# Kernel optimization log

Hardware: AMD Instinct MI355X
Metric: run time of the kernel (lower is better)

The kernel has to match this reference:

```python
import jax, jax.numpy as jnp
import numpy as np

N_AGENTS, RNN_H, N_HEADS, GAT_D, EMB, SDIM = 16, 64, 4, 32, 32, 128


def setup_inputs() -> dict:
    key = jax.random.key(0)
    ks = jax.random.split(key, 16)
    xav = lambda k, shp: jax.random.normal(k, shp, jnp.float32) * (2.0 / sum(shp)) ** 0.5
    return {
        'agent_qs': jax.random.normal(ks[0], (32, 128, N_AGENTS), jnp.float32),
        'states': jax.random.normal(ks[1], (32, 128, SDIM), jnp.float32),
        'hidden_states': jax.random.normal(ks[2], (32, 128, N_AGENTS, RNN_H), jnp.float32),
        'uncertainty': jax.random.uniform(ks[3], (32, 128, 1), jnp.float32),
        'W_gat': xav(ks[4], (RNN_H, N_HEADS * GAT_D)) * 1.414,
        'att_a': xav(ks[5], (1, N_HEADS, 2 * GAT_D)) * 1.414,
        'w1s_W': xav(ks[6], (SDIM + 1, N_HEADS * EMB * GAT_D)),
        'w1s_b': jnp.zeros((N_HEADS * EMB * GAT_D,), jnp.float32),
        'b1_W': xav(ks[7], (SDIM, EMB)),
        'b1_b': jnp.zeros((EMB,), jnp.float32),
        'wf_W': xav(ks[8], (SDIM, EMB)),
        'wf_b': jnp.zeros((EMB,), jnp.float32),
        'V1_W': xav(ks[9], (SDIM, EMB)),
        'V1_b': jnp.zeros((EMB,), jnp.float32),
        'V2_W': xav(ks[10], (EMB, 1)),
        'V2_b': jnp.zeros((1,), jnp.float32),
    }


def gat(h, W_gat, att_a):
    B, n, _ = h.shape
    hp = (h @ W_gat).reshape(B, n, N_HEADS, GAT_D).transpose(0, 2, 1, 3)  # (B,H,n,d)
    a_src, a_dst = att_a[0, :, :GAT_D], att_a[0, :, GAT_D:]  # (H,d) each
    # e[b,h,i,j] = <hp_i, a_src> + <hp_j, a_dst>  (same math as concat+dot)
    src = jnp.einsum('bhnd,hd->bhn', hp, a_src)
    dst = jnp.einsum('bhnd,hd->bhn', hp, a_dst)
    e = jax.nn.leaky_relu(src[:, :, :, None] + dst[:, :, None, :], 0.2)
    attn = jax.nn.softmax(e, axis=-1)
    return jax.nn.elu(jnp.einsum('bhij,bhjd->bhid', attn, hp))  # (B,H,n,d)


def reference(agent_qs, states, hidden_states, uncertainty, W_gat, att_a,
              w1s_W, w1s_b, b1_W, b1_b, wf_W, wf_b, V1_W, V1_b, V2_W, V2_b):
    bs = agent_qs.shape[0]
    s = states.reshape(-1, SDIM)                      # (B,S)
    qs = agent_qs.reshape(-1, 1, N_AGENTS)            # (B,1,n)
    hs = hidden_states.reshape(-1, N_AGENTS, RNN_H)   # (B,n,R)
    unc = uncertainty.reshape(-1, 1)
    s_aug = jnp.concatenate([s, unc], axis=1)         # (B,S+1)

    g = gat(hs, W_gat, att_a)                         # (B,H,n,d)

    w1_state = (s_aug @ w1s_W + w1s_b).reshape(-1, N_HEADS, EMB, GAT_D)
    w1_heads = jnp.abs(jnp.einsum('bhed,bhnd->bhen', w1_state, g))  # (B,H,E,n)
    w1 = w1_heads.mean(axis=1).transpose(0, 2, 1)     # (B,n,E)

    b1 = (s @ b1_W + b1_b)[:, None, :]                # (B,1,E)
    hidden = jax.nn.elu(jnp.einsum('bin,bne->bie', qs, w1) + b1)  # (B,1,E)

    w_final = jnp.abs(s @ wf_W + wf_b)[:, :, None]    # (B,E,1)
    v = (jax.nn.relu(s @ V1_W + V1_b) @ V2_W + V2_b)[:, None, :]  # (B,1,1)
    y = jnp.einsum('bie,bej->bij', hidden, w_final) + v
    return y.reshape(bs, -1, 1)
```

## Files before the change

kernel.cpp:

```cpp
#include <hip/hip_runtime.h>
#include <math.h>


typedef __attribute__((ext_vector_type(8))) short short8;
typedef __attribute__((ext_vector_type(8))) unsigned short ushort8;
typedef __attribute__((ext_vector_type(4))) unsigned short ushort4v;
typedef __attribute__((ext_vector_type(4))) float float4v;
typedef __attribute__((ext_vector_type(4))) _Float16 half4v;

static __device__ inline unsigned short f2bf(float f) {
    unsigned int x;
    __builtin_memcpy(&x, &f, 4);
    unsigned int r = x + 0x7fffu + ((x >> 16) & 1u);
    return (unsigned short)(r >> 16);
}

static __device__ inline short8 pack8(float4 f0, float4 f1) {
    ushort8 o;
    o[0] = f2bf(f0.x); o[1] = f2bf(f0.y); o[2] = f2bf(f0.z); o[3] = f2bf(f0.w);
    o[4] = f2bf(f1.x); o[5] = f2bf(f1.y); o[6] = f2bf(f1.z); o[7] = f2bf(f1.w);
    short8 s;
    __builtin_memcpy(&s, &o, 16);
    return s;
}

__global__ __launch_bounds__(256) void k0_prep(
    const float* __restrict__ w1s_W,
    const float* __restrict__ W_gat,
    const float* __restrict__ att_a,
    const float* __restrict__ states,
    const float* __restrict__ b1_W, const float* __restrict__ b1_b,
    const float* __restrict__ wf_W, const float* __restrict__ wf_b,
    const float* __restrict__ V1_W, const float* __restrict__ V1_b,
    const float* __restrict__ V2_W, const float* __restrict__ V2_b,
    unsigned short* __restrict__ w1sTf,
    unsigned short* __restrict__ WgTf,
    float* __restrict__ b1v, float* __restrict__ wfv,
    float* __restrict__ out)
{
    __shared__ __align__(16) char SMEM[49152];
    const int tid = threadIdx.x, bx = blockIdx.x;

    if (bx < 256) {
        unsigned short* T = (unsigned short*)SMEM;
        const int c0 = bx * 16;
        const int cc = tid & 15, kr = tid >> 4;
        #pragma unroll
        for (int t = 0; t < 8; ++t) {
            int k = t * 16 + kr;
            T[cc * 136 + k] = f2bf(w1s_W[(size_t)k * 4096 + c0 + cc]);
        }
        __syncthreads();
        const int ks = tid >> 6, q = (tid >> 4) & 3, mm = tid & 15;
        *(ushort8*)&w1sTf[(size_t)bx * 2048 + tid * 8] =
            *(const ushort8*)&T[mm * 136 + ks * 32 + q * 8];
    } else if (bx == 256) {
        unsigned short* T = (unsigned short*)SMEM;
        #pragma unroll
        for (int t = 0; t < 32; ++t) {
            int i = t * 256 + tid;
            int k = i >> 7, c = i & 127;
            T[c * 72 + k] = f2bf(W_gat[k * 128 + c]);
        }
        __syncthreads();
        #pragma unroll
        for (int t = 0; t < 4; ++t) {
            int i = t * 256 + tid;
            int nt = i >> 7, w = i & 127;
            int kh = w >> 6, q = (w >> 4) & 3, mm = w & 15;
            *(ushort8*)&WgTf[nt * 1024 + w * 8] =
                *(const ushort8*)&T[(nt * 16 + mm) * 72 + kh * 32 + q * 8];
        }
        {
            const int k = tid >> 2, h = tid & 3;
            float ss = 0.f, dd = 0.f;
            #pragma unroll
            for (int d = 0; d < 32; ++d) {
                float wv = W_gat[k * 128 + h * 32 + d];
                ss = fmaf(wv, att_a[h * 64 + d], ss);
                dd = fmaf(wv, att_a[h * 64 + 32 + d], dd);
            }
            const int base = 8192 + (k >> 5) * 512 + ((k >> 3) & 3) * 128 + (k & 7);
            WgTf[base + h * 8]       = f2bf(ss);
            WgTf[base + (4 + h) * 8] = f2bf(dd);
        }
        #pragma unroll
        for (int t = 0; t < 2; ++t) {
            int i = t * 256 + tid;
            int kh = i >> 8, q = (i >> 6) & 3, mm = 8 + ((i >> 3) & 7), j = i & 7;
            WgTf[8192 + kh * 512 + q * 128 + mm * 8 + j] = 0;
        }
    } else {
        float* WL = (float*)SMEM;
        for (int i = tid; i < 12288; i += 256)
            WL[i] = (i < 4096) ? b1_W[i] : (i < 8192 ? wf_W[i - 4096] : V1_W[i - 8192]);
        __syncthreads();

        const int wave = tid >> 6, lane = tid & 63, mm = lane & 15, q = lane >> 4;
        const int b0w = (bx - 257) * 64 + wave * 16;

        short8 a[4];
        #pragma unroll
        for (int ks = 0; ks < 4; ++ks) {
            const float* sp = states + (size_t)(b0w + mm) * 128 + ks * 32 + q * 8;
            a[ks] = pack8(*(const float4*)sp, *(const float4*)(sp + 4));
        }
        float4v accT[6];
        #pragma unroll
        for (int nt = 0; nt < 6; ++nt) accT[nt] = (float4v){0.f, 0.f, 0.f, 0.f};
        #pragma unroll
        for (int nt = 0; nt < 6; ++nt) {
            const int set = nt >> 1, e = (nt & 1) * 16 + mm;
            #pragma unroll
            for (int ks = 0; ks < 4; ++ks) {
                ushort8 bfu;
                #pragma unroll
                for (int j = 0; j < 8; ++j)
                    bfu[j] = f2bf(WL[set * 4096 + (ks * 32 + q * 8 + j) * 32 + e]);
                short8 bf;
                __builtin_memcpy(&bf, &bfu, 16);
                accT[nt] = __builtin_amdgcn_mfma_f32_16x16x32_bf16(a[ks], bf, accT[nt], 0, 0, 0);
            }
        }
        float vsum[4] = {0.f, 0.f, 0.f, 0.f};
        #pragma unroll
        for (int p = 0; p < 2; ++p) {
            const int e = p * 16 + mm;
            const float bb1 = b1_b[e], bwf = wf_b[e], bv1 = V1_b[e], v2 = V2_W[e];
            #pragma unroll
            for (int reg = 0; reg < 4; ++reg) {
                const int row = b0w + q * 4 + reg;
                b1v[(size_t)row * 32 + e] = accT[p][reg] + bb1;
                wfv[(size_t)row * 32 + e] = fabsf(accT[2 + p][reg] + bwf);
                vsum[reg] += fmaxf(accT[4 + p][reg] + bv1, 0.f) * v2;
            }
        }
        #pragma unroll
        for (int reg = 0; reg < 4; ++reg) {
            vsum[reg] += __shfl_xor(vsum[reg], 1);
            vsum[reg] += __shfl_xor(vsum[reg], 2);
            vsum[reg] += __shfl_xor(vsum[reg], 4);
            vsum[reg] += __shfl_xor(vsum[reg], 8);
        }
        if (mm == 0) {
            #pragma unroll
            for (int reg = 0; reg < 4; ++reg)
                out[b0w + q * 4 + reg] = vsum[reg] + V2_b[0];
        }
    }
}

__global__ __launch_bounds__(256) void k1_gat(
    const float* __restrict__ hidden_states,
    const unsigned short* __restrict__ WgTf,
    unsigned short* __restrict__ g_bf)
{
    const int wave = threadIdx.x >> 6;
    const int b = blockIdx.x * 4 + wave;
    const int lane = threadIdx.x & 63, m = lane & 15, quad = lane >> 4;
    __shared__ __align__(16) float sc[4 * 320];
    float* scr = &sc[wave * 320];

    const float* hrow = hidden_states + ((size_t)b * 16 + m) * 64;
    float4 f0 = *(const float4*)(hrow + quad * 8);
    float4 f1 = *(const float4*)(hrow + quad * 8 + 4);
    short8 a0 = pack8(f0, f1);
    f0 = *(const float4*)(hrow + 32 + quad * 8);
    f1 = *(const float4*)(hrow + 32 + quad * 8 + 4);
    short8 a1 = pack8(f0, f1);

    float4v hpt[9];
    #pragma unroll
    for (int nt = 0; nt < 9; ++nt) {
        short8 bf0 = *(const short8*)&WgTf[nt * 1024 + lane * 8];
        short8 bf1 = *(const short8*)&WgTf[nt * 1024 + 512 + lane * 8];
        float4v z = (float4v){0.f, 0.f, 0.f, 0.f};
        z = __builtin_amdgcn_mfma_f32_16x16x32_bf16(a0, bf0, z, 0, 0, 0);
        z = __builtin_amdgcn_mfma_f32_16x16x32_bf16(a1, bf1, z, 0, 0, 0);
        hpt[nt] = z;
    }

    {
        float4 pr = {hpt[8][0], hpt[8][1], hpt[8][2], hpt[8][3]};
        *(float4*)&scr[m * 20 + quad * 4] = pr;
    }

    #pragma unroll
    for (int h = 0; h < 4; ++h) {
        const float src_m = scr[h * 20 + m];
        float4 pdv = *(const float4*)&scr[(4 + h) * 20 + quad * 4];
        float pd[4] = {pdv.x, pdv.y, pdv.z, pdv.w};

        float e_[4];
        #pragma unroll
        for (int jj = 0; jj < 4; ++jj) {
            float x = src_m + pd[jj];
            e_[jj] = fmaxf(x, 0.2f * x);
        }
        float mx = fmaxf(fmaxf(e_[0], e_[1]), fmaxf(e_[2], e_[3]));
        mx = fmaxf(mx, __shfl_xor(mx, 16));
        mx = fmaxf(mx, __shfl_xor(mx, 32));
        float p_[4], ssum = 0.f;
        #pragma unroll
        for (int jj = 0; jj < 4; ++jj) { p_[jj] = __expf(e_[jj] - mx); ssum += p_[jj]; }
        ssum += __shfl_xor(ssum, 16);
        ssum += __shfl_xor(ssum, 32);
        const float inv = __builtin_amdgcn_rcpf(ssum);

        half4v bfrag;
        #pragma unroll
        for (int jj = 0; jj < 4; ++jj) bfrag[jj] = (_Float16)(p_[jj] * inv);

        #pragma unroll
        for (int p = 0; p < 2; ++p) {
            float4v ct = hpt[2 * h + p];
            half4v afrag;
            #pragma unroll
            for (int t = 0; t < 4; ++t) afrag[t] = (_Float16)ct[t];
            float4v z = (float4v){0.f, 0.f, 0.f, 0.f};
            z = __builtin_amdgcn_mfma_f32_16x16x16f16(afrag, bfrag, z, 0, 0, 0);
            ushort4v o;
            #pragma unroll
            for (int t = 0; t < 4; ++t) {
                float x = z[t];
                float ex = __expf(x) - 1.f;
                x = (x > 0.f) ? x : ex;
                o[t] = f2bf(x);
            }
            *(ushort4v*)&g_bf[((size_t)b * 4 + h) * 512 + m * 32 + p * 16 + quad * 4] = o;
        }
    }
}

__global__ __launch_bounds__(256) void k2_mix(
    const float* __restrict__ states,
    const unsigned short* __restrict__ w1sTf,
    const unsigned short* __restrict__ g_bf,
    const float* __restrict__ agent_qs,
    const float* __restrict__ uncertainty,
    const float* __restrict__ w1s_W,
    const float* __restrict__ w1s_b,
    const float* __restrict__ b1v, const float* __restrict__ wfv,
    float* __restrict__ out)
{
    const int r0 = blockIdx.x * 16;
    const int eg = blockIdx.y;
    const int wave = threadIdx.x >> 6;
    const int lane = threadIdx.x & 63, m = lane & 15, quad = lane >> 4;
    __shared__ __align__(16) unsigned short Wt[2][16 * 328];

    short8 a[4];
    #pragma unroll
    for (int ks = 0; ks < 4; ++ks) {
        const float* sp = states + (size_t)(r0 + m) * 128 + ks * 32 + quad * 8;
        a[ks] = pack8(*(const float4*)sp, *(const float4*)(sp + 4));
    }
    float us[4];
    #pragma unroll
    for (int reg = 0; reg < 4; ++reg)
        us[reg] = uncertainty[r0 + quad * 4 + reg];
    float qs_r[4];
    #pragma unroll
    for (int rr = 0; rr < 4; ++rr)
        qs_r[rr] = agent_qs[(r0 + wave * 4 + rr) * 16 + m];

    const float* w128 = w1s_W + (size_t)128 * 4096;
    float Sacc[4][4] = {};

    #pragma unroll
    for (int h = 0; h < 4; ++h) {
        unsigned short* buf = &Wt[h & 1][0];

        #pragma unroll
        for (int t = 0; t < 4; ++t) {
            const int ctl = wave * 4 + t;
            const int ct = h * 64 + eg * 16 + ctl;
            const int c_loc = ctl * 16 + m;
            const int cg = h * 1024 + eg * 256 + c_loc;
            const float wfix = w128[cg], bias = w1s_b[cg];
            float4v acc = (float4v){0.f, 0.f, 0.f, 0.f};
            #pragma unroll
            for (int ks = 0; ks < 4; ++ks) {
                short8 bfr = *(const short8*)&w1sTf[(size_t)ct * 2048 + ks * 512 + lane * 8];
                acc = __builtin_amdgcn_mfma_f32_16x16x32_bf16(a[ks], bfr, acc, 0, 0, 0);
            }
            const int el = c_loc >> 5, d = c_loc & 31;
            #pragma unroll
            for (int reg = 0; reg < 4; ++reg)
                buf[(quad * 4 + reg) * 328 + el * 40 + d] =
                    f2bf(acc[reg] + us[reg] * wfix + bias);
        }

        short8 gf[4];
        #pragma unroll
        for (int rr = 0; rr < 4; ++rr)
            gf[rr] = *(const short8*)&g_bf[((size_t)(r0 + wave * 4 + rr) * 4 + h) * 512 + m * 32 + quad * 8];

        __syncthreads();

        #pragma unroll
        for (int rr = 0; rr < 4; ++rr) {
            const int r = wave * 4 + rr;
            short8 af = *(const short8*)&buf[r * 328 + (m & 7) * 40 + quad * 8];
            float4v z = (float4v){0.f, 0.f, 0.f, 0.f};
            z = __builtin_amdgcn_mfma_f32_16x16x32_bf16(af, gf[rr], z, 0, 0, 0);
            #pragma unroll
            for (int reg = 0; reg < 4; ++reg)
                Sacc[rr][reg] += fabsf(z[reg]);
        }
    }

    #pragma unroll
    for (int rr = 0; rr < 4; ++rr) {
        const int r = r0 + wave * 4 + rr;
        float sn[4];
        #pragma unroll
        for (int reg = 0; reg < 4; ++reg) sn[reg] = Sacc[rr][reg] * qs_r[rr];
        #pragma unroll
        for (int mask = 1; mask <= 8; mask <<= 1) {
            #pragma unroll
            for (int reg = 0; reg < 4; ++reg) sn[reg] += __shfl_xor(sn[reg], mask);
        }
        const float* bb = &b1v[(size_t)r * 32 + eg * 8 + (quad & 1) * 4];
        const float* ww = &wfv[(size_t)r * 32 + eg * 8 + (quad & 1) * 4];
        float4 b4 = *(const float4*)bb;
        float4 w4 = *(const float4*)ww;
        float bq[4] = {b4.x, b4.y, b4.z, b4.w};
        float wq[4] = {w4.x, w4.y, w4.z, w4.w};
        float local = 0.f;
        #pragma unroll
        for (int reg = 0; reg < 4; ++reg) {
            float hid = 0.25f * sn[reg] + bq[reg];
            hid = (hid > 0.f) ? hid : expm1f(hid);
            local = fmaf(hid, wq[reg], local);
        }
        local += __shfl_xor(local, 16);
        if (lane == 0) atomicAdd(&out[r], local);
    }
}

extern "C" void kernel_launch(void* const* d_in, const int* in_sizes, int n_in,
                              void* d_out, int out_size, void* d_ws, size_t ws_size,
                              hipStream_t stream)
{
    const float* agent_qs      = (const float*)d_in[0];
    const float* states        = (const float*)d_in[1];
    const float* hidden_states = (const float*)d_in[2];
    const float* uncertainty   = (const float*)d_in[3];
    const float* W_gat         = (const float*)d_in[4];
    const float* att_a         = (const float*)d_in[5];
    const float* w1s_W         = (const float*)d_in[6];
    const float* w1s_b         = (const float*)d_in[7];
    const float* b1_W          = (const float*)d_in[8];
    const float* b1_b          = (const float*)d_in[9];
    const float* wf_W          = (const float*)d_in[10];
    const float* wf_b          = (const float*)d_in[11];
    const float* V1_W          = (const float*)d_in[12];
    const float* V1_b          = (const float*)d_in[13];
    const float* V2_W          = (const float*)d_in[14];
    const float* V2_b          = (const float*)d_in[15];

    char* w = (char*)d_ws;
    unsigned short* w1sTf   = (unsigned short*)w;  w += (size_t)524288 * 2;
    unsigned short* WgTf    = (unsigned short*)w;  w += (size_t)9216 * 2;
    unsigned short* g_bf    = (unsigned short*)w;  w += (size_t)8388608 * 2;
    float* b1v              = (float*)w;           w += (size_t)131072 * 4;
    float* wfv              = (float*)w;           w += (size_t)131072 * 4;
    float* out              = (float*)d_out;

    k0_prep<<<321, 256, 0, stream>>>(w1s_W, W_gat, att_a, states,
                                     b1_W, b1_b, wf_W, wf_b, V1_W, V1_b,
                                     V2_W, V2_b, w1sTf, WgTf, b1v, wfv, out);

    k1_gat<<<1024, 256, 0, stream>>>(hidden_states, WgTf, g_bf);

    dim3 gmix(256, 4);
    k2_mix<<<gmix, 256, 0, stream>>>(states, w1sTf, g_bf, agent_qs, uncertainty,
                                     w1s_W, w1s_b, b1v, wfv, out);
}
```

Baseline: 136.5 us.

## Pack bf16 conversions, pre-convert prep weights, and split mix kernel into eight groups

Swaps the scalar bf16 rounding for packed float2-to-bf162 conversions in pack8 and the GAT output, and writes 16-byte stores of the interleaved head output. The prep kernel now stores the small state weights in LDS already converted to bf16 with a padded stride, so each MFMA B fragment no longer reconverts. The mix kernel goes from 4 to 8 embedding groups per row block, each wave computing two column tiles with a smaller LDS buffer, which doubles grid parallelism but also doubles the reloads of states, g_bf and the atomic adds.

```diff
diff --git a/kernel.cpp b/kernel.cpp
--- a/kernel.cpp
+++ b/kernel.cpp
@@ -1,10 +1,10 @@
 #include <hip/hip_runtime.h>
+#include <hip/hip_bf16.h>
 #include <math.h>
 
 
 typedef __attribute__((ext_vector_type(8))) short short8;
 typedef __attribute__((ext_vector_type(8))) unsigned short ushort8;
-typedef __attribute__((ext_vector_type(4))) unsigned short ushort4v;
 typedef __attribute__((ext_vector_type(4))) float float4v;
 typedef __attribute__((ext_vector_type(4))) _Float16 half4v;
 
@@ -15,12 +15,18 @@
     return (unsigned short)(r >> 16);
 }
 
+static __device__ inline unsigned int cvtpk(float lo, float hi) {
+    __hip_bfloat162 h = __float22bfloat162_rn(make_float2(lo, hi));
+    unsigned int u;
+    __builtin_memcpy(&u, &h, 4);
+    return u;
+}
+
 static __device__ inline short8 pack8(float4 f0, float4 f1) {
-    ushort8 o;
-    o[0] = f2bf(f0.x); o[1] = f2bf(f0.y); o[2] = f2bf(f0.z); o[3] = f2bf(f0.w);
-    o[4] = f2bf(f1.x); o[5] = f2bf(f1.y); o[6] = f2bf(f1.z); o[7] = f2bf(f1.w);
+    unsigned int u[4] = {cvtpk(f0.x, f0.y), cvtpk(f0.z, f0.w),
+                         cvtpk(f1.x, f1.y), cvtpk(f1.z, f1.w)};
     short8 s;
-    __builtin_memcpy(&s, &o, 16);
+    __builtin_memcpy(&s, u, 16);
     return s;
 }
 
@@ -38,7 +44,7 @@
     float* __restrict__ b1v, float* __restrict__ wfv,
     float* __restrict__ out)
 {
-    __shared__ __align__(16) char SMEM[49152];
+    __shared__ __align__(16) char SMEM[26112];
     const int tid = threadIdx.x, bx = blockIdx.x;
 
     if (bx < 256) {
@@ -91,9 +97,12 @@
             WgTf[8192 + kh * 512 + q * 128 + mm * 8 + j] = 0;
         }
     } else {
-        float* WL = (float*)SMEM;
-        for (int i = tid; i < 12288; i += 256)
-            WL[i] = (i < 4096) ? b1_W[i] : (i < 8192 ? wf_W[i - 4096] : V1_W[i - 8192]);
+        unsigned short* WLu = (unsigned short*)SMEM;
+        for (int i = tid; i < 12288; i += 256) {
+            float v = (i < 4096) ? b1_W[i] : (i < 8192 ? wf_W[i - 4096] : V1_W[i - 8192]);
+            int set = i >> 12, k = (i >> 5) & 127, e = i & 31;
+            WLu[set * 4352 + k * 34 + e] = f2bf(v);
+        }
         __syncthreads();
 
         const int wave = tid >> 6, lane = tid & 63, mm = lane & 15, q = lane >> 4;
@@ -116,7 +125,7 @@
                 ushort8 bfu;
                 #pragma unroll
                 for (int j = 0; j < 8; ++j)
-                    bfu[j] = f2bf(WL[set * 4096 + (ks * 32 + q * 8 + j) * 32 + e]);
+                    bfu[j] = WLu[set * 4352 + (ks * 32 + q * 8 + j) * 34 + e];
                 short8 bf;
                 __builtin_memcpy(&bf, &bfu, 16);
                 accT[nt] = __builtin_amdgcn_mfma_f32_16x16x32_bf16(a[ks], bf, accT[nt], 0, 0, 0);
@@ -211,6 +220,7 @@
         #pragma unroll
         for (int jj = 0; jj < 4; ++jj) bfrag[jj] = (_Float16)(p_[jj] * inv);
 
+        float4v zp[2];
         #pragma unroll
         for (int p = 0; p < 2; ++p) {
             float4v ct = hpt[2 * h + p];
@@ -218,17 +228,20 @@
             #pragma unroll
             for (int t = 0; t < 4; ++t) afrag[t] = (_Float16)ct[t];
             float4v z = (float4v){0.f, 0.f, 0.f, 0.f};
-            z = __builtin_amdgcn_mfma_f32_16x16x16f16(afrag, bfrag, z, 0, 0, 0);
-            ushort4v o;
-            #pragma unroll
-            for (int t = 0; t < 4; ++t) {
-                float x = z[t];
-                float ex = __expf(x) - 1.f;
-                x = (x > 0.f) ? x : ex;
-                o[t] = f2bf(x);
-            }
-            *(ushort4v*)&g_bf[((size_t)b * 4 + h) * 512 + m * 32 + p * 16 + quad * 4] = o;
-        }
+            zp[p] = __builtin_amdgcn_mfma_f32_16x16x16f16(afrag, bfrag, z, 0, 0, 0);
+        }
+        unsigned int w[4];
+        #pragma unroll
+        for (int t = 0; t < 4; ++t) {
+            float x0 = zp[0][t];
+            x0 = (x0 > 0.f) ? x0 : (__expf(x0) - 1.f);
+            float x1 = zp[1][t];
+            x1 = (x1 > 0.f) ? x1 : (__expf(x1) - 1.f);
+            w[t] = cvtpk(x0, x1);
+        }
+        short8 o8;
+        __builtin_memcpy(&o8, w, 16);
+        *(short8*)&g_bf[((size_t)b * 4 + h) * 512 + m * 32 + quad * 8] = o8;
     }
 }
 
@@ -247,7 +260,7 @@
     const int eg = blockIdx.y;
     const int wave = threadIdx.x >> 6;
     const int lane = threadIdx.x & 63, m = lane & 15, quad = lane >> 4;
-    __shared__ __align__(16) unsigned short Wt[2][16 * 328];
+    __shared__ __align__(16) unsigned short Wt[2][16 * 168];
 
     short8 a[4];
     #pragma unroll
@@ -271,24 +284,30 @@
     for (int h = 0; h < 4; ++h) {
         unsigned short* buf = &Wt[h & 1][0];
 
-        #pragma unroll
-        for (int t = 0; t < 4; ++t) {
-            const int ctl = wave * 4 + t;
-            const int ct = h * 64 + eg * 16 + ctl;
+        float4v acc0, acc1;
+        #pragma unroll
+        for (int t = 0; t < 2; ++t) {
+            const int ctl = wave * 2 + t;
+            const int ct = h * 64 + eg * 8 + ctl;
             const int c_loc = ctl * 16 + m;
-            const int cg = h * 1024 + eg * 256 + c_loc;
+            const int cg = h * 1024 + eg * 128 + c_loc;
             const float wfix = w128[cg], bias = w1s_b[cg];
-            float4v acc = (float4v){0.f, 0.f, 0.f, 0.f};
+            float4v z = (float4v){0.f, 0.f, 0.f, 0.f};
             #pragma unroll
             for (int ks = 0; ks < 4; ++ks) {
                 short8 bfr = *(const short8*)&w1sTf[(size_t)ct * 2048 + ks * 512 + lane * 8];
-                acc = __builtin_amdgcn_mfma_f32_16x16x32_bf16(a[ks], bfr, acc, 0, 0, 0);
+                z = __builtin_amdgcn_mfma_f32_16x16x32_bf16(a[ks], bfr, z, 0, 0, 0);
             }
-            const int el = c_loc >> 5, d = c_loc & 31;
             #pragma unroll
             for (int reg = 0; reg < 4; ++reg)
-                buf[(quad * 4 + reg) * 328 + el * 40 + d] =
-                    f2bf(acc[reg] + us[reg] * wfix + bias);
+                z[reg] = z[reg] + us[reg] * wfix + bias;
+            if (t == 0) acc0 = z; else acc1 = z;
+        }
+        #pragma unroll
+        for (int reg = 0; reg < 4; ++reg) {
+            const int row = quad * 4 + reg;
+            unsigned int pair = cvtpk(acc0[reg], acc1[reg]);
+            *(unsigned int*)&buf[row * 168 + wave * 40 + 2 * m] = pair;
         }
 
         short8 gf[4];
@@ -301,7 +320,7 @@
         #pragma unroll
         for (int rr = 0; rr < 4; ++rr) {
             const int r = wave * 4 + rr;
-            short8 af = *(const short8*)&buf[r * 328 + (m & 7) * 40 + quad * 8];
+            short8 af = *(const short8*)&buf[r * 168 + (m & 3) * 40 + quad * 8];
             float4v z = (float4v){0.f, 0.f, 0.f, 0.f};
             z = __builtin_amdgcn_mfma_f32_16x16x32_bf16(af, gf[rr], z, 0, 0, 0);
             #pragma unroll
@@ -321,10 +340,8 @@
             #pragma unroll
             for (int reg = 0; reg < 4; ++reg) sn[reg] += __shfl_xor(sn[reg], mask);
         }
-        const float* bb = &b1v[(size_t)r * 32 + eg * 8 + (quad & 1) * 4];
-        const float* ww = &wfv[(size_t)r * 32 + eg * 8 + (quad & 1) * 4];
-        float4 b4 = *(const float4*)bb;
-        float4 w4 = *(const float4*)ww;
+        float4 b4 = *(const float4*)&b1v[(size_t)r * 32 + eg * 4];
+        float4 w4 = *(const float4*)&wfv[(size_t)r * 32 + eg * 4];
         float bq[4] = {b4.x, b4.y, b4.z, b4.w};
         float wq[4] = {w4.x, w4.y, w4.z, w4.w};
         float local = 0.f;
@@ -334,7 +351,6 @@
             hid = (hid > 0.f) ? hid : expm1f(hid);
             local = fmaf(hid, wq[reg], local);
         }
-        local += __shfl_xor(local, 16);
         if (lane == 0) atomicAdd(&out[r], local);
     }
 }
@@ -374,7 +390,7 @@
 
     k1_gat<<<1024, 256, 0, stream>>>(hidden_states, WgTf, g_bf);
 
-    dim3 gmix(256, 4);
+    dim3 gmix(256, 8);
     k2_mix<<<gmix, 256, 0, stream>>>(states, w1sTf, g_bf, agent_qs, uncertainty,
                                      w1s_W, w1s_b, b1v, wfv, out);
 }
```

New measurement: 151.6 us. +11.1%, slower.
